# Kernel tuning notes

Hardware: AMD Instinct MI355X
Metric: run time of the kernel (lower is better)

## Reference

```python
import jax, jax.numpy as jnp
import numpy as np

N = 50000
E = 400000
NFEAT = 256
NHID = 64
HEADS = [4, 4, 4]
NCLASS = 121
NEG_SLOPE = 0.2


def gat_conv(h, W, al, ar, src, dst, H, D):
    # h: [N, F_in], W: [F_in, H*D], al/ar: [H, D]
    feat = (h @ W).reshape(N, H, D)                    # [N, H, D]
    el = jnp.sum(feat * al[None], axis=-1)             # [N, H]
    er = jnp.sum(feat * ar[None], axis=-1)             # [N, H]
    e = jax.nn.leaky_relu(el[src] + er[dst], NEG_SLOPE)  # [E, H]
    # edge softmax over incoming edges of each dst node
    m = jax.ops.segment_max(e, dst, num_segments=N)    # [N, H]
    ex = jnp.exp(e - m[dst])                           # [E, H]
    s = jax.ops.segment_sum(ex, dst, num_segments=N)   # [N, H]
    alpha = ex / s[dst]                                # [E, H]
    msg = alpha[..., None] * feat[src]                 # [E, H, D]
    return jax.ops.segment_sum(msg, dst, num_segments=N)  # [N, H, D]


def setup_inputs() -> dict:
    key = jax.random.key(0)
    ks = jax.random.split(key, 12)
    d = {
        "h": jax.random.normal(ks[0], (N, NFEAT), dtype=jnp.float32),
        "src": jax.random.randint(ks[1], (E,), 0, N),
        "dst": jax.random.randint(ks[2], (E,), 0, N),
        "W1": jax.random.normal(ks[3], (NFEAT, HEADS[0] * NHID), dtype=jnp.float32) * 0.05,
        "al1": jax.random.normal(ks[4], (HEADS[0], NHID), dtype=jnp.float32) * 0.1,
        "ar1": jax.random.normal(ks[5], (HEADS[0], NHID), dtype=jnp.float32) * 0.1,
        "W2": jax.random.normal(ks[6], (HEADS[0] * NHID, HEADS[1] * NHID), dtype=jnp.float32) * 0.05,
        "al2": jax.random.normal(ks[7], (HEADS[1], NHID), dtype=jnp.float32) * 0.1,
        "ar2": jax.random.normal(ks[8], (HEADS[1], NHID), dtype=jnp.float32) * 0.1,
        "W3": jax.random.normal(ks[9], (HEADS[1] * NHID, HEADS[2] * NCLASS), dtype=jnp.float32) * 0.05,
        "al3": jax.random.normal(ks[10], (HEADS[2], NCLASS), dtype=jnp.float32) * 0.1,
        "ar3": jax.random.normal(ks[11], (HEADS[2], NCLASS), dtype=jnp.float32) * 0.1,
    }
    return d


def reference(h, src, dst, W1, al1, ar1, W2, al2, ar2, W3, al3, ar3):
    # layer 1: [N, H0, NHID] -> flatten -> ELU (norm='none', drop=0, residual='none')
    x = gat_conv(h, W1, al1, ar1, src, dst, HEADS[0], NHID).reshape(N, -1)
    x = jax.nn.elu(x)
    # layer 2
    x = gat_conv(x, W2, al2, ar2, src, dst, HEADS[1], NHID).reshape(N, -1)
    x = jax.nn.elu(x)
    # output layer: mean over heads
    x = gat_conv(x, W3, al3, ar3, src, dst, HEADS[2], NCLASS).mean(axis=1)
    return x
```

## Files before the change

### kernel.cpp

```cpp
#include <hip/hip_runtime.h>
#include <cstddef>

#define NN 50000
#define NE 400000
#define NH 4
#define NC 121
#define MAXSLOT 600000

typedef __attribute__((ext_vector_type(8))) short short8;
typedef __attribute__((ext_vector_type(4))) float f32x4;

static __device__ __forceinline__ unsigned short f2bf(float f) {
    unsigned u = __float_as_uint(f);
    u += 0x7fffu + ((u >> 16) & 1u);
    return (unsigned short)(u >> 16);
}
static __device__ __forceinline__ float bf2f(unsigned short u) {
    return __uint_as_float(((unsigned)u) << 16);
}

__global__ __launch_bounds__(256) void cast_x(const float* __restrict__ in,
                                              unsigned short* __restrict__ out, int n4) {
    int i = blockIdx.x * blockDim.x + threadIdx.x;
    if (i >= n4) return;
    float4 v = *(const float4*)&in[i * 4];
    ushort4 o;
    o.x = f2bf(v.x); o.y = f2bf(v.y); o.z = f2bf(v.z); o.w = f2bf(v.w);
    *(ushort4*)&out[i * 4] = o;
}

__global__ __launch_bounds__(256) void cast_BT(const float* __restrict__ B,
                                               unsigned short* __restrict__ BT,
                                               int N, int Npad) {
    int i = blockIdx.x * blockDim.x + threadIdx.x;
    if (i >= Npad * 256) return;
    int n = i >> 8, k = i & 255;
    float v = (n < N) ? B[(size_t)k * N + n] : 0.f;
    BT[i] = f2bf(v);
}

__global__ __launch_bounds__(256) void cast_BTcat(const float* __restrict__ W3,
                                                  unsigned short* __restrict__ BT) {
    int i = blockIdx.x * blockDim.x + threadIdx.x;
    if (i >= 128 * 1024) return;
    int c = i >> 10, kk = i & 1023;
    int h = kk >> 8, k = kk & 255;
    float v = (c < NC) ? 0.25f * W3[(size_t)k * 484 + h * NC + c] : 0.f;
    BT[i] = f2bf(v);
}

__global__ __launch_bounds__(256) void wvec3_k(const float* __restrict__ W3,
                                               const float* __restrict__ al3,
                                               const float* __restrict__ ar3,
                                               float* __restrict__ wl3,
                                               float* __restrict__ wr3) {
    int i = blockIdx.x * blockDim.x + threadIdx.x;
    if (i >= 2048) return;
    int j = i & 1023;
    int h = j >> 8, k = j & 255;
    const float* a = (i < 1024) ? al3 : ar3;
    const float* wrow = W3 + (size_t)k * 484 + h * NC;
    const float* arow = a + h * NC;
    float s = 0.f;
    for (int d = 0; d < NC; ++d) s += wrow[d] * arow[d];
    if (i < 1024) wl3[j] = s; else wr3[j] = s;
}

__global__ __launch_bounds__(256) void gemm_bf16(const unsigned short* __restrict__ A,
                                                 const unsigned short* __restrict__ BT,
                                                 float* __restrict__ Cf,
                                                 unsigned short* __restrict__ Cb,
                                                 int M, int Nout, int K) {
    __shared__ __align__(16) unsigned short Alds[128 * 32];
    __shared__ __align__(16) unsigned short Blds[128 * 32];
    const int tid = threadIdx.x;
    const int wave = tid >> 6;
    const int lane = tid & 63;
    const int quad = lane >> 4;
    const int ml = lane & 15;
    const int m0 = blockIdx.x * 128;
    const int n0 = blockIdx.y * 128;
    const int wm0 = (wave >> 1) * 64;
    const int wn0 = (wave & 1) * 64;
    const int r = tid >> 2;
    const int c8 = (tid & 3) * 8;

    f32x4 acc[4][4] = {};

    for (int k0 = 0; k0 < K; k0 += 32) {
        #pragma unroll
        for (int p = 0; p < 2; ++p) {
            int rr = r + p * 64;
            int m = m0 + rr;
            uint4 va = make_uint4(0u, 0u, 0u, 0u);
            if (m < M) va = *(const uint4*)&A[(size_t)m * K + k0 + c8];
            *(uint4*)&Alds[rr * 32 + c8] = va;
            int n = n0 + rr;
            uint4 vb = *(const uint4*)&BT[(size_t)n * K + k0 + c8];
            *(uint4*)&Blds[rr * 32 + c8] = vb;
        }
        __syncthreads();

        short8 af[4], bf[4];
        #pragma unroll
        for (int i = 0; i < 4; ++i)
            af[i] = *(const short8*)&Alds[(wm0 + i * 16 + ml) * 32 + quad * 8];
        #pragma unroll
        for (int j = 0; j < 4; ++j)
            bf[j] = *(const short8*)&Blds[(wn0 + j * 16 + ml) * 32 + quad * 8];
        #pragma unroll
        for (int i = 0; i < 4; ++i)
            #pragma unroll
            for (int j = 0; j < 4; ++j)
                acc[i][j] = __builtin_amdgcn_mfma_f32_16x16x32_bf16(af[i], bf[j], acc[i][j], 0, 0, 0);
        __syncthreads();
    }

    #pragma unroll
    for (int i = 0; i < 4; ++i) {
        #pragma unroll
        for (int reg = 0; reg < 4; ++reg) {
            int m = m0 + wm0 + i * 16 + quad * 4 + reg;
            if (m >= M) continue;
            #pragma unroll
            for (int j = 0; j < 4; ++j) {
                int n = n0 + wn0 + j * 16 + ml;
                if (n < Nout) {
                    if (Cb) Cb[(size_t)m * Nout + n] = f2bf(acc[i][j][reg]);
                    else    Cf[(size_t)m * Nout + n] = acc[i][j][reg];
                }
            }
        }
    }
}

__global__ __launch_bounds__(256) void node_attn(const unsigned short* __restrict__ feat,
                                                 const float* __restrict__ al,
                                                 const float* __restrict__ ar,
                                                 float* __restrict__ el,
                                                 float* __restrict__ er) {
    int wid = (blockIdx.x * blockDim.x + threadIdx.x) >> 6;
    int lane = threadIdx.x & 63;
    if (wid >= NN) return;
    int h = lane >> 4;
    int dl = (lane & 15) * 4;
    ushort4 xv = *(const ushort4*)&feat[(size_t)wid * 256 + lane * 4];
    float4 a4 = *(const float4*)&al[h * 64 + dl];
    float4 r4 = *(const float4*)&ar[h * 64 + dl];
    float f0 = bf2f(xv.x), f1 = bf2f(xv.y), f2 = bf2f(xv.z), f3 = bf2f(xv.w);
    float sl = f0 * a4.x + f1 * a4.y + f2 * a4.z + f3 * a4.w;
    float sr = f0 * r4.x + f1 * r4.y + f2 * r4.z + f3 * r4.w;
    #pragma unroll
    for (int off = 8; off; off >>= 1) {
        sl += __shfl_xor(sl, off);
        sr += __shfl_xor(sr, off);
    }
    if ((lane & 15) == 0) {
        el[wid * 4 + h] = sl;
        er[wid * 4 + h] = sr;
    }
}

__global__ __launch_bounds__(256) void elr3_k(const unsigned short* __restrict__ x,
                                              const float* __restrict__ wl3,
                                              const float* __restrict__ wr3,
                                              float* __restrict__ el,
                                              float* __restrict__ er) {
    int wid = (blockIdx.x * blockDim.x + threadIdx.x) >> 6;
    int lane = threadIdx.x & 63;
    if (wid >= NN) return;
    ushort4 xv = *(const ushort4*)&x[(size_t)wid * 256 + lane * 4];
    float f[4] = {bf2f(xv.x), bf2f(xv.y), bf2f(xv.z), bf2f(xv.w)};
    float sl[4] = {}, sr[4] = {};
    #pragma unroll
    for (int h = 0; h < 4; ++h) {
        float4 a4 = *(const float4*)&wl3[h * 256 + lane * 4];
        float4 r4 = *(const float4*)&wr3[h * 256 + lane * 4];
        sl[h] = f[0] * a4.x + f[1] * a4.y + f[2] * a4.z + f[3] * a4.w;
        sr[h] = f[0] * r4.x + f[1] * r4.y + f[2] * r4.z + f[3] * r4.w;
    }
    #pragma unroll
    for (int off = 32; off; off >>= 1) {
        #pragma unroll
        for (int h = 0; h < 4; ++h) {
            sl[h] += __shfl_xor(sl[h], off);
            sr[h] += __shfl_xor(sr[h], off);
        }
    }
    if (lane == 0) {
        #pragma unroll
        for (int h = 0; h < 4; ++h) {
            el[wid * 4 + h] = sl[h];
            er[wid * 4 + h] = sr[h];
        }
    }
}

__global__ __launch_bounds__(256) void hist_k(const int* __restrict__ dst, int* __restrict__ deg) {
    int e = blockIdx.x * blockDim.x + threadIdx.x;
    if (e < NE) atomicAdd(&deg[dst[e]], 1);
}

__global__ __launch_bounds__(256) void scan1(const int* __restrict__ deg,
                                             int* __restrict__ excl,
                                             int* __restrict__ partials) {
    __shared__ int sh[256];
    int i = blockIdx.x * 256 + threadIdx.x;
    int v = (i < NN) ? ((deg[i] + 3) & ~3) : 0;
    sh[threadIdx.x] = v;
    __syncthreads();
    for (int off = 1; off < 256; off <<= 1) {
        int t = (threadIdx.x >= off) ? sh[threadIdx.x - off] : 0;
        __syncthreads();
        sh[threadIdx.x] += t;
        __syncthreads();
    }
    if (i < NN) excl[i] = sh[threadIdx.x] - v;
    if (threadIdx.x == 255) partials[blockIdx.x] = sh[255];
}

__global__ __launch_bounds__(256) void scan2(int* __restrict__ partials, int nb) {
    __shared__ int sh[256];
    int t = threadIdx.x;
    int v = (t < nb) ? partials[t] : 0;
    sh[t] = v;
    __syncthreads();
    for (int off = 1; off < 256; off <<= 1) {
        int x = (t >= off) ? sh[t - off] : 0;
        __syncthreads();
        sh[t] += x;
        __syncthreads();
    }
    if (t < nb) partials[t] = sh[t] - v;
}

__global__ __launch_bounds__(256) void scan3(const int* __restrict__ excl,
                                             const int* __restrict__ partials,
                                             int* __restrict__ rowptr) {
    int i = blockIdx.x * 256 + threadIdx.x;
    if (i < NN) rowptr[i] = excl[i] + partials[blockIdx.x];
}

__global__ __launch_bounds__(256) void scatter_k(const int* __restrict__ src,
                                                 const int* __restrict__ dst,
                                                 const int* __restrict__ rowptr,
                                                 int* __restrict__ cursor,
                                                 int* __restrict__ ssrc,
                                                 int* __restrict__ sdst) {
    int e = blockIdx.x * blockDim.x + threadIdx.x;
    if (e >= NE) return;
    int d = dst[e];
    int p = atomicAdd(&cursor[d], 1);
    int pos = rowptr[d] + p;
    ssrc[pos] = src[e];
    sdst[pos] = d;
}

__global__ __launch_bounds__(256) void edgew_k(const int* __restrict__ ssrc,
                                               const int* __restrict__ sdst,
                                               const float* __restrict__ el,
                                               const float* __restrict__ er,
                                               float* __restrict__ wcsr) {
    int i = blockIdx.x * blockDim.x + threadIdx.x;
    if (i >= MAXSLOT) return;
    int d = sdst[i];
    float w0 = 0.f, w1 = 0.f, w2 = 0.f, w3 = 0.f;
    if (d >= 0) {
        int s = ssrc[i];
        float4 e_l = *(const float4*)&el[s * 4];
        float4 e_r = *(const float4*)&er[d * 4];
        float v0 = e_l.x + e_r.x; v0 = v0 > 0.f ? v0 : 0.2f * v0;
        float v1 = e_l.y + e_r.y; v1 = v1 > 0.f ? v1 : 0.2f * v1;
        float v2 = e_l.z + e_r.z; v2 = v2 > 0.f ? v2 : 0.2f * v2;
        float v3 = e_l.w + e_r.w; v3 = v3 > 0.f ? v3 : 0.2f * v3;
        w0 = __expf(v0); w1 = __expf(v1); w2 = __expf(v2); w3 = __expf(v3);
    }
    wcsr[0 * MAXSLOT + i] = w0;
    wcsr[1 * MAXSLOT + i] = w1;
    wcsr[2 * MAXSLOT + i] = w2;
    wcsr[3 * MAXSLOT + i] = w3;
}

__global__ __launch_bounds__(256) void agg256(const int* __restrict__ rowptr,
                                              const int* __restrict__ deg,
                                              const int* __restrict__ ssrc,
                                              const float* __restrict__ wcsr,
                                              const unsigned short* __restrict__ feat,
                                              unsigned short* __restrict__ ybf) {
    int wid = (blockIdx.x * blockDim.x + threadIdx.x) >> 6;
    int lane = threadIdx.x & 63;
    if (wid >= NN) return;
    int n = wid;
    int start = rowptr[n];
    int cnt4 = (deg[n] + 3) & ~3;
    int head = lane >> 4;
    const float* wch = wcsr + (size_t)head * MAXSLOT;
    float ax = 0.f, ay = 0.f, az = 0.f, aw = 0.f, ssum = 0.f;
    for (int k = 0; k < cnt4; k += 4) {
        int4 sv = *(const int4*)&ssrc[start + k];
        float4 w4 = *(const float4*)&wch[start + k];
        ushort4 f0 = *(const ushort4*)&feat[(size_t)sv.x * 256 + lane * 4];
        ushort4 f1 = *(const ushort4*)&feat[(size_t)sv.y * 256 + lane * 4];
        ushort4 f2 = *(const ushort4*)&feat[(size_t)sv.z * 256 + lane * 4];
        ushort4 f3 = *(const ushort4*)&feat[(size_t)sv.w * 256 + lane * 4];
        ssum += (w4.x + w4.y) + (w4.z + w4.w);
        ax += w4.x * bf2f(f0.x) + w4.y * bf2f(f1.x) + w4.z * bf2f(f2.x) + w4.w * bf2f(f3.x);
        ay += w4.x * bf2f(f0.y) + w4.y * bf2f(f1.y) + w4.z * bf2f(f2.y) + w4.w * bf2f(f3.y);
        az += w4.x * bf2f(f0.z) + w4.y * bf2f(f1.z) + w4.z * bf2f(f2.z) + w4.w * bf2f(f3.z);
        aw += w4.x * bf2f(f0.w) + w4.y * bf2f(f1.w) + w4.z * bf2f(f2.w) + w4.w * bf2f(f3.w);
    }
    float inv = ssum > 0.f ? 1.0f / ssum : 0.f;
    ax *= inv; ay *= inv; az *= inv; aw *= inv;
    ax = ax > 0.f ? ax : (__expf(ax) - 1.f);
    ay = ay > 0.f ? ay : (__expf(ay) - 1.f);
    az = az > 0.f ? az : (__expf(az) - 1.f);
    aw = aw > 0.f ? aw : (__expf(aw) - 1.f);
    ushort4 o;
    o.x = f2bf(ax); o.y = f2bf(ay); o.z = f2bf(az); o.w = f2bf(aw);
    *(ushort4*)&ybf[(size_t)n * 256 + lane * 4] = o;
}

__global__ __launch_bounds__(256) void agg3(const int* __restrict__ rowptr,
                                            const int* __restrict__ deg,
                                            const int* __restrict__ ssrc,
                                            const float* __restrict__ wcsr,
                                            const unsigned short* __restrict__ x,
                                            unsigned short* __restrict__ xagg) {
    int wid = (blockIdx.x * blockDim.x + threadIdx.x) >> 6;
    int lane = threadIdx.x & 63;
    if (wid >= NN) return;
    int n = wid;
    int start = rowptr[n];
    int cnt4 = (deg[n] + 3) & ~3;
    float acc[4][4] = {};
    float ssum[4] = {};
    for (int k = 0; k < cnt4; k += 4) {
        int4 sv = *(const int4*)&ssrc[start + k];
        float4 w0 = *(const float4*)&wcsr[0 * MAXSLOT + start + k];
        float4 w1 = *(const float4*)&wcsr[1 * MAXSLOT + start + k];
        float4 w2 = *(const float4*)&wcsr[2 * MAXSLOT + start + k];
        float4 w3 = *(const float4*)&wcsr[3 * MAXSLOT + start + k];
        ushort4 xa = *(const ushort4*)&x[(size_t)sv.x * 256 + lane * 4];
        ushort4 xb = *(const ushort4*)&x[(size_t)sv.y * 256 + lane * 4];
        ushort4 xc = *(const ushort4*)&x[(size_t)sv.z * 256 + lane * 4];
        ushort4 xd = *(const ushort4*)&x[(size_t)sv.w * 256 + lane * 4];
        ssum[0] += (w0.x + w0.y) + (w0.z + w0.w);
        ssum[1] += (w1.x + w1.y) + (w1.z + w1.w);
        ssum[2] += (w2.x + w2.y) + (w2.z + w2.w);
        ssum[3] += (w3.x + w3.y) + (w3.z + w3.w);
        float fa[4] = {bf2f(xa.x), bf2f(xa.y), bf2f(xa.z), bf2f(xa.w)};
        float fb[4] = {bf2f(xb.x), bf2f(xb.y), bf2f(xb.z), bf2f(xb.w)};
        float fc[4] = {bf2f(xc.x), bf2f(xc.y), bf2f(xc.z), bf2f(xc.w)};
        float fd[4] = {bf2f(xd.x), bf2f(xd.y), bf2f(xd.z), bf2f(xd.w)};
        #pragma unroll
        for (int d = 0; d < 4; ++d) {
            acc[0][d] += w0.x * fa[d] + w0.y * fb[d] + w0.z * fc[d] + w0.w * fd[d];
            acc[1][d] += w1.x * fa[d] + w1.y * fb[d] + w1.z * fc[d] + w1.w * fd[d];
            acc[2][d] += w2.x * fa[d] + w2.y * fb[d] + w2.z * fc[d] + w2.w * fd[d];
            acc[3][d] += w3.x * fa[d] + w3.y * fb[d] + w3.z * fc[d] + w3.w * fd[d];
        }
    }
    #pragma unroll
    for (int h = 0; h < 4; ++h) {
        float inv = ssum[h] > 0.f ? 1.f / ssum[h] : 0.f;
        ushort4 o;
        o.x = f2bf(acc[h][0] * inv); o.y = f2bf(acc[h][1] * inv);
        o.z = f2bf(acc[h][2] * inv); o.w = f2bf(acc[h][3] * inv);
        *(ushort4*)&xagg[(size_t)n * 1024 + h * 256 + lane * 4] = o;
    }
}

extern "C" void kernel_launch(void* const* d_in, const int* in_sizes, int n_in,
                              void* d_out, int out_size, void* d_ws, size_t ws_size,
                              hipStream_t stream) {
    const float* h   = (const float*)d_in[0];
    const int*   src = (const int*)d_in[1];
    const int*   dst = (const int*)d_in[2];
    const float* W1  = (const float*)d_in[3];
    const float* al1 = (const float*)d_in[4];
    const float* ar1 = (const float*)d_in[5];
    const float* W2  = (const float*)d_in[6];
    const float* al2 = (const float*)d_in[7];
    const float* ar2 = (const float*)d_in[8];
    const float* W3  = (const float*)d_in[9];
    const float* al3 = (const float*)d_in[10];
    const float* ar3 = (const float*)d_in[11];
    float* out = (float*)d_out;

    float* ws = (float*)d_ws;
    unsigned short* x_bf    = (unsigned short*)ws;
    unsigned short* h_bf    = (unsigned short*)(ws + 6400000);
    unsigned short* feat_bf = (unsigned short*)(ws + 12800000);
    unsigned short* xagg    = (unsigned short*)(ws + 6400000);
    float* el  = ws + 32000000;
    float* er  = ws + 32200000;
    float* wl3 = ws + 32400000;
    float* wr3 = ws + 32401024;
    unsigned short* BT1   = (unsigned short*)(ws + 32402048);
    unsigned short* BT2   = (unsigned short*)(ws + 32434816);
    unsigned short* BTcat = (unsigned short*)(ws + 32467584);
    float* wcsr = ws + 32533120;
    int* ibase  = (int*)(ws + 34933120);
    int* deg      = ibase;
    int* excl     = ibase + 50000;
    int* partials = ibase + 100000;
    int* rowptr   = ibase + 100256;
    int* cursor   = ibase + 150256;
    int* ssrc     = ibase + 200256;
    int* sdst     = ibase + 800256;

    const int NB = (NN + 255) / 256;
    const int SLOT_BLOCKS = (MAXSLOT + 255) / 256;

    hipMemsetAsync(deg, 0, NN * sizeof(int), stream);
    hipMemsetAsync(cursor, 0, NN * sizeof(int), stream);
    hipMemsetAsync(ssrc, 0, MAXSLOT * sizeof(int), stream);
    hipMemsetAsync(sdst, 0xFF, MAXSLOT * sizeof(int), stream);
    hist_k<<<(NE + 255) / 256, 256, 0, stream>>>(dst, deg);
    scan1<<<NB, 256, 0, stream>>>(deg, excl, partials);
    scan2<<<1, 256, 0, stream>>>(partials, NB);
    scan3<<<NB, 256, 0, stream>>>(excl, partials, rowptr);
    scatter_k<<<(NE + 255) / 256, 256, 0, stream>>>(src, dst, rowptr, cursor, ssrc, sdst);

    cast_x<<<(NN * 256 / 4 + 255) / 256, 256, 0, stream>>>(h, h_bf, NN * 256 / 4);
    cast_BT<<<(256 * 256 + 255) / 256, 256, 0, stream>>>(W1, BT1, 256, 256);
    cast_BT<<<(256 * 256 + 255) / 256, 256, 0, stream>>>(W2, BT2, 256, 256);
    cast_BTcat<<<512, 256, 0, stream>>>(W3, BTcat);
    wvec3_k<<<8, 256, 0, stream>>>(W3, al3, ar3, wl3, wr3);

    dim3 g256((NN + 127) / 128, 2);
    dim3 gOut((NN + 127) / 128, 1);
    const int WAVE_BLOCKS = (NN * 64 + 255) / 256;

    gemm_bf16<<<g256, 256, 0, stream>>>(h_bf, BT1, nullptr, feat_bf, NN, 256, 256);
    node_attn<<<WAVE_BLOCKS, 256, 0, stream>>>(feat_bf, al1, ar1, el, er);
    edgew_k<<<SLOT_BLOCKS, 256, 0, stream>>>(ssrc, sdst, el, er, wcsr);
    agg256<<<WAVE_BLOCKS, 256, 0, stream>>>(rowptr, deg, ssrc, wcsr, feat_bf, x_bf);

    gemm_bf16<<<g256, 256, 0, stream>>>(x_bf, BT2, nullptr, feat_bf, NN, 256, 256);
    node_attn<<<WAVE_BLOCKS, 256, 0, stream>>>(feat_bf, al2, ar2, el, er);
    edgew_k<<<SLOT_BLOCKS, 256, 0, stream>>>(ssrc, sdst, el, er, wcsr);
    agg256<<<WAVE_BLOCKS, 256, 0, stream>>>(rowptr, deg, ssrc, wcsr, feat_bf, x_bf);

    elr3_k<<<WAVE_BLOCKS, 256, 0, stream>>>(x_bf, wl3, wr3, el, er);
    edgew_k<<<SLOT_BLOCKS, 256, 0, stream>>>(ssrc, sdst, el, er, wcsr);
    agg3<<<WAVE_BLOCKS, 256, 0, stream>>>(rowptr, deg, ssrc, wcsr, x_bf, xagg);
    gemm_bf16<<<gOut, 256, 0, stream>>>(xagg, BTcat, out, nullptr, NN, NC, 1024);
}
```

Measured before the change: 456.6 us.

## Fuse node attention into GEMM epilogue and split aggregation across two waves

New measurement: 487.4 us. 1.07x slower.

```diff
diff --git a/kernel.cpp b/kernel.cpp
--- a/kernel.cpp
+++ b/kernel.cpp
@@ -70,6 +70,10 @@
                                                  const unsigned short* __restrict__ BT,
                                                  float* __restrict__ Cf,
                                                  unsigned short* __restrict__ Cb,
+                                                 const float* __restrict__ al,
+                                                 const float* __restrict__ ar,
+                                                 float* __restrict__ el,
+                                                 float* __restrict__ er,
                                                  int M, int Nout, int K) {
     __shared__ __align__(16) unsigned short Alds[128 * 32];
     __shared__ __align__(16) unsigned short Blds[128 * 32];
@@ -132,32 +136,38 @@
             }
         }
     }
-}
-
-__global__ __launch_bounds__(256) void node_attn(const unsigned short* __restrict__ feat,
-                                                 const float* __restrict__ al,
-                                                 const float* __restrict__ ar,
-                                                 float* __restrict__ el,
-                                                 float* __restrict__ er) {
-    int wid = (blockIdx.x * blockDim.x + threadIdx.x) >> 6;
-    int lane = threadIdx.x & 63;
-    if (wid >= NN) return;
-    int h = lane >> 4;
-    int dl = (lane & 15) * 4;
-    ushort4 xv = *(const ushort4*)&feat[(size_t)wid * 256 + lane * 4];
-    float4 a4 = *(const float4*)&al[h * 64 + dl];
-    float4 r4 = *(const float4*)&ar[h * 64 + dl];
-    float f0 = bf2f(xv.x), f1 = bf2f(xv.y), f2 = bf2f(xv.z), f3 = bf2f(xv.w);
-    float sl = f0 * a4.x + f1 * a4.y + f2 * a4.z + f3 * a4.w;
-    float sr = f0 * r4.x + f1 * r4.y + f2 * r4.z + f3 * r4.w;
-    #pragma unroll
-    for (int off = 8; off; off >>= 1) {
-        sl += __shfl_xor(sl, off);
-        sr += __shfl_xor(sr, off);
-    }
-    if ((lane & 15) == 0) {
-        el[wid * 4 + h] = sl;
-        er[wid * 4 + h] = sr;
+
+    if (el) {
+        int head = (n0 + wn0) >> 6;
+        float alv[4], arv[4];
+        #pragma unroll
+        for (int j = 0; j < 4; ++j) {
+            alv[j] = al[head * 64 + j * 16 + ml];
+            arv[j] = ar[head * 64 + j * 16 + ml];
+        }
+        #pragma unroll
+        for (int i = 0; i < 4; ++i) {
+            #pragma unroll
+            for (int reg = 0; reg < 4; ++reg) {
+                float sl = 0.f, sr = 0.f;
+                #pragma unroll
+                for (int j = 0; j < 4; ++j) {
+                    float v = acc[i][j][reg];
+                    sl += v * alv[j];
+                    sr += v * arv[j];
+                }
+                #pragma unroll
+                for (int off = 1; off < 16; off <<= 1) {
+                    sl += __shfl_xor(sl, off);
+                    sr += __shfl_xor(sr, off);
+                }
+                int m = m0 + wm0 + i * 16 + quad * 4 + reg;
+                if (ml == 0 && m < M) {
+                    el[m * 4 + head] = sl;
+                    er[m * 4 + head] = sr;
+                }
+            }
+        }
     }
 }
 
@@ -287,37 +297,34 @@
                                               const float* __restrict__ wcsr,
                                               const unsigned short* __restrict__ feat,
                                               unsigned short* __restrict__ ybf) {
-    int wid = (blockIdx.x * blockDim.x + threadIdx.x) >> 6;
+    int gid = (blockIdx.x * blockDim.x + threadIdx.x) >> 6;
     int lane = threadIdx.x & 63;
-    if (wid >= NN) return;
-    int n = wid;
+    if (gid >= NN * 2) return;
+    int n = gid >> 1, half = gid & 1;
+    int g = half * 128 + lane * 2;
+    int head = g >> 6;
     int start = rowptr[n];
     int cnt4 = (deg[n] + 3) & ~3;
-    int head = lane >> 4;
     const float* wch = wcsr + (size_t)head * MAXSLOT;
-    float ax = 0.f, ay = 0.f, az = 0.f, aw = 0.f, ssum = 0.f;
+    float a0 = 0.f, a1 = 0.f, ssum = 0.f;
     for (int k = 0; k < cnt4; k += 4) {
         int4 sv = *(const int4*)&ssrc[start + k];
         float4 w4 = *(const float4*)&wch[start + k];
-        ushort4 f0 = *(const ushort4*)&feat[(size_t)sv.x * 256 + lane * 4];
-        ushort4 f1 = *(const ushort4*)&feat[(size_t)sv.y * 256 + lane * 4];
-        ushort4 f2 = *(const ushort4*)&feat[(size_t)sv.z * 256 + lane * 4];
-        ushort4 f3 = *(const ushort4*)&feat[(size_t)sv.w * 256 + lane * 4];
+        ushort2 f0 = *(const ushort2*)&feat[(size_t)sv.x * 256 + g];
+        ushort2 f1 = *(const ushort2*)&feat[(size_t)sv.y * 256 + g];
+        ushort2 f2 = *(const ushort2*)&feat[(size_t)sv.z * 256 + g];
+        ushort2 f3 = *(const ushort2*)&feat[(size_t)sv.w * 256 + g];
         ssum += (w4.x + w4.y) + (w4.z + w4.w);
-        ax += w4.x * bf2f(f0.x) + w4.y * bf2f(f1.x) + w4.z * bf2f(f2.x) + w4.w * bf2f(f3.x);
-        ay += w4.x * bf2f(f0.y) + w4.y * bf2f(f1.y) + w4.z * bf2f(f2.y) + w4.w * bf2f(f3.y);
-        az += w4.x * bf2f(f0.z) + w4.y * bf2f(f1.z) + w4.z * bf2f(f2.z) + w4.w * bf2f(f3.z);
-        aw += w4.x * bf2f(f0.w) + w4.y * bf2f(f1.w) + w4.z * bf2f(f2.w) + w4.w * bf2f(f3.w);
+        a0 += w4.x * bf2f(f0.x) + w4.y * bf2f(f1.x) + w4.z * bf2f(f2.x) + w4.w * bf2f(f3.x);
+        a1 += w4.x * bf2f(f0.y) + w4.y * bf2f(f1.y) + w4.z * bf2f(f2.y) + w4.w * bf2f(f3.y);
     }
     float inv = ssum > 0.f ? 1.0f / ssum : 0.f;
-    ax *= inv; ay *= inv; az *= inv; aw *= inv;
-    ax = ax > 0.f ? ax : (__expf(ax) - 1.f);
-    ay = ay > 0.f ? ay : (__expf(ay) - 1.f);
-    az = az > 0.f ? az : (__expf(az) - 1.f);
-    aw = aw > 0.f ? aw : (__expf(aw) - 1.f);
-    ushort4 o;
-    o.x = f2bf(ax); o.y = f2bf(ay); o.z = f2bf(az); o.w = f2bf(aw);
-    *(ushort4*)&ybf[(size_t)n * 256 + lane * 4] = o;
+    a0 *= inv; a1 *= inv;
+    a0 = a0 > 0.f ? a0 : (__expf(a0) - 1.f);
+    a1 = a1 > 0.f ? a1 : (__expf(a1) - 1.f);
+    ushort2 o;
+    o.x = f2bf(a0); o.y = f2bf(a1);
+    *(ushort2*)&ybf[(size_t)n * 256 + g] = o;
 }
 
 __global__ __launch_bounds__(256) void agg3(const int* __restrict__ rowptr,
@@ -326,13 +333,14 @@
                                             const float* __restrict__ wcsr,
                                             const unsigned short* __restrict__ x,
                                             unsigned short* __restrict__ xagg) {
-    int wid = (blockIdx.x * blockDim.x + threadIdx.x) >> 6;
+    int gid = (blockIdx.x * blockDim.x + threadIdx.x) >> 6;
     int lane = threadIdx.x & 63;
-    if (wid >= NN) return;
-    int n = wid;
+    if (gid >= NN * 2) return;
+    int n = gid >> 1, half = gid & 1;
+    int g = half * 128 + lane * 2;
     int start = rowptr[n];
     int cnt4 = (deg[n] + 3) & ~3;
-    float acc[4][4] = {};
+    float acc[4][2] = {};
     float ssum[4] = {};
     for (int k = 0; k < cnt4; k += 4) {
         int4 sv = *(const int4*)&ssrc[start + k];
@@ -340,33 +348,34 @@
         float4 w1 = *(const float4*)&wcsr[1 * MAXSLOT + start + k];
         float4 w2 = *(const float4*)&wcsr[2 * MAXSLOT + start + k];
         float4 w3 = *(const float4*)&wcsr[3 * MAXSLOT + start + k];
-        ushort4 xa = *(const ushort4*)&x[(size_t)sv.x * 256 + lane * 4];
-        ushort4 xb = *(const ushort4*)&x[(size_t)sv.y * 256 + lane * 4];
-        ushort4 xc = *(const ushort4*)&x[(size_t)sv.z * 256 + lane * 4];
-        ushort4 xd = *(const ushort4*)&x[(size_t)sv.w * 256 + lane * 4];
+        ushort2 xa = *(const ushort2*)&x[(size_t)sv.x * 256 + g];
+        ushort2 xb = *(const ushort2*)&x[(size_t)sv.y * 256 + g];
+        ushort2 xc = *(const ushort2*)&x[(size_t)sv.z * 256 + g];
+        ushort2 xd = *(const ushort2*)&x[(size_t)sv.w * 256 + g];
         ssum[0] += (w0.x + w0.y) + (w0.z + w0.w);
         ssum[1] += (w1.x + w1.y) + (w1.z + w1.w);
         ssum[2] += (w2.x + w2.y) + (w2.z + w2.w);
         ssum[3] += (w3.x + w3.y) + (w3.z + w3.w);
-        float fa[4] = {bf2f(xa.x), bf2f(xa.y), bf2f(xa.z), bf2f(xa.w)};
-        float fb[4] = {bf2f(xb.x), bf2f(xb.y), bf2f(xb.z), bf2f(xb.w)};
-        float fc[4] = {bf2f(xc.x), bf2f(xc.y), bf2f(xc.z), bf2f(xc.w)};
-        float fd[4] = {bf2f(xd.x), bf2f(xd.y), bf2f(xd.z), bf2f(xd.w)};
-        #pragma unroll
-        for (int d = 0; d < 4; ++d) {
-            acc[0][d] += w0.x * fa[d] + w0.y * fb[d] + w0.z * fc[d] + w0.w * fd[d];
-            acc[1][d] += w1.x * fa[d] + w1.y * fb[d] + w1.z * fc[d] + w1.w * fd[d];
-            acc[2][d] += w2.x * fa[d] + w2.y * fb[d] + w2.z * fc[d] + w2.w * fd[d];
-            acc[3][d] += w3.x * fa[d] + w3.y * fb[d] + w3.z * fc[d] + w3.w * fd[d];
-        }
+        float fa0 = bf2f(xa.x), fa1 = bf2f(xa.y);
+        float fb0 = bf2f(xb.x), fb1 = bf2f(xb.y);
+        float fc0 = bf2f(xc.x), fc1 = bf2f(xc.y);
+        float fd0 = bf2f(xd.x), fd1 = bf2f(xd.y);
+        acc[0][0] += w0.x * fa0 + w0.y * fb0 + w0.z * fc0 + w0.w * fd0;
+        acc[0][1] += w0.x * fa1 + w0.y * fb1 + w0.z * fc1 + w0.w * fd1;
+        acc[1][0] += w1.x * fa0 + w1.y * fb0 + w1.z * fc0 + w1.w * fd0;
+        acc[1][1] += w1.x * fa1 + w1.y * fb1 + w1.z * fc1 + w1.w * fd1;
+        acc[2][0] += w2.x * fa0 + w2.y * fb0 + w2.z * fc0 + w2.w * fd0;
+        acc[2][1] += w2.x * fa1 + w2.y * fb1 + w2.z * fc1 + w2.w * fd1;
+        acc[3][0] += w3.x * fa0 + w3.y * fb0 + w3.z * fc0 + w3.w * fd0;
+        acc[3][1] += w3.x * fa1 + w3.y * fb1 + w3.z * fc1 + w3.w * fd1;
     }
     #pragma unroll
     for (int h = 0; h < 4; ++h) {
         float inv = ssum[h] > 0.f ? 1.f / ssum[h] : 0.f;
-        ushort4 o;
-        o.x = f2bf(acc[h][0] * inv); o.y = f2bf(acc[h][1] * inv);
-        o.z = f2bf(acc[h][2] * inv); o.w = f2bf(acc[h][3] * inv);
-        *(ushort4*)&xagg[(size_t)n * 1024 + h * 256 + lane * 4] = o;
+        ushort2 o;
+        o.x = f2bf(acc[h][0] * inv);
+        o.y = f2bf(acc[h][1] * inv);
+        *(ushort2*)&xagg[(size_t)n * 1024 + h * 256 + g] = o;
     }
 }
 
@@ -430,20 +439,19 @@
 
     dim3 g256((NN + 127) / 128, 2);
     dim3 gOut((NN + 127) / 128, 1);
-    const int WAVE_BLOCKS = (NN * 64 + 255) / 256;
-
-    gemm_bf16<<<g256, 256, 0, stream>>>(h_bf, BT1, nullptr, feat_bf, NN, 256, 256);
-    node_attn<<<WAVE_BLOCKS, 256, 0, stream>>>(feat_bf, al1, ar1, el, er);
+    const int WAVE_BLOCKS  = (NN * 64 + 255) / 256;
+    const int AGG_BLOCKS   = (NN * 2 * 64 + 255) / 256;
+
+    gemm_bf16<<<g256, 256, 0, stream>>>(h_bf, BT1, nullptr, feat_bf, al1, ar1, el, er, NN, 256, 256);
     edgew_k<<<SLOT_BLOCKS, 256, 0, stream>>>(ssrc, sdst, el, er, wcsr);
-    agg256<<<WAVE_BLOCKS, 256, 0, stream>>>(rowptr, deg, ssrc, wcsr, feat_bf, x_bf);
-
-    gemm_bf16<<<g256, 256, 0, stream>>>(x_bf, BT2, nullptr, feat_bf, NN, 256, 256);
-    node_attn<<<WAVE_BLOCKS, 256, 0, stream>>>(feat_bf, al2, ar2, el, er);
+    agg256<<<AGG_BLOCKS, 256, 0, stream>>>(rowptr, deg, ssrc, wcsr, feat_bf, x_bf);
+
+    gemm_bf16<<<g256, 256, 0, stream>>>(x_bf, BT2, nullptr, feat_bf, al2, ar2, el, er, NN, 256, 256);
     edgew_k<<<SLOT_BLOCKS, 256, 0, stream>>>(ssrc, sdst, el, er, wcsr);
-    agg256<<<WAVE_BLOCKS, 256, 0, stream>>>(rowptr, deg, ssrc, wcsr, feat_bf, x_bf);
+    agg256<<<AGG_BLOCKS, 256, 0, stream>>>(rowptr, deg, ssrc, wcsr, feat_bf, x_bf);
 
     elr3_k<<<WAVE_BLOCKS, 256, 0, stream>>>(x_bf, wl3, wr3, el, er);
     edgew_k<<<SLOT_BLOCKS, 256, 0, stream>>>(ssrc, sdst, el, er, wcsr);
-    agg3<<<WAVE_BLOCKS, 256, 0, stream>>>(rowptr, deg, ssrc, wcsr, x_bf, xagg);
-    gemm_bf16<<<gOut, 256, 0, stream>>>(xagg, BTcat, out, nullptr, NN, NC, 1024);
-}
+    agg3<<<AGG_BLOCKS, 256, 0, stream>>>(rowptr, deg, ssrc, wcsr, x_bf, xagg);
+    gemm_bf16<<<gOut, 256, 0, stream>>>(xagg, BTcat, out, nullptr, nullptr, nullptr, nullptr, nullptr, NN, NC, 1024);
+}
```
